# Performance work log

Hardware: AMD Instinct MI355X
Metric: run time of the kernel (lower is better)

## Reference

```python
import jax, jax.numpy as jnp
import numpy as np

NEG_SLOPE = 0.2

def edge_softmax(logits, dst, num_nodes):
    # logits: [E, H]; softmax over incoming edges of each dst node, per head
    m = jax.ops.segment_max(logits, dst, num_segments=num_nodes)  # [N, H]
    e = jnp.exp(logits - m[dst])
    s = jax.ops.segment_sum(e, dst, num_segments=num_nodes)  # [N, H]
    return e / s[dst]

def gat_layer(h, src, dst, W, al, ar, b, activation):
    # W: [F_in, H*D], al/ar: [H, D], b: [H, D]
    N = h.shape[0]
    H, D = al.shape
    feat = (h @ W).reshape(N, H, D)
    el = jnp.sum(feat * al, axis=-1)  # [N, H]
    er = jnp.sum(feat * ar, axis=-1)  # [N, H]
    e = jax.nn.leaky_relu(el[src] + er[dst], NEG_SLOPE)  # [E, H]
    a = edge_softmax(e, dst, N)  # [E, H]
    msg = feat[src] * a[:, :, None]  # [E, H, D]
    rst = jax.ops.segment_sum(msg, dst, num_segments=N) + b[None]  # [N, H, D]
    if activation:
        rst = jax.nn.relu(rst)
    return rst

def setup_inputs() -> dict:
    key = jax.random.key(0)
    ks = jax.random.split(key, 16)
    N, E = 50000, 800000
    IN, HID, OUT, H = 128, 64, 64, 4
    s = 0.1
    return {
        "features": jax.random.normal(ks[0], (N, IN), jnp.float32),
        "src": jax.random.randint(ks[1], (E,), 0, N),
        "dst": jax.random.randint(ks[2], (E,), 0, N),
        "W1": jax.random.normal(ks[3], (IN, H * HID), jnp.float32) * s,
        "al1": jax.random.normal(ks[4], (H, HID), jnp.float32) * s,
        "ar1": jax.random.normal(ks[5], (H, HID), jnp.float32) * s,
        "b1": jnp.zeros((H, HID), jnp.float32),
        "W2": jax.random.normal(ks[6], (H * HID, H * HID), jnp.float32) * s,
        "al2": jax.random.normal(ks[7], (H, HID), jnp.float32) * s,
        "ar2": jax.random.normal(ks[8], (H, HID), jnp.float32) * s,
        "b2": jnp.zeros((H, HID), jnp.float32),
        "W3": jax.random.normal(ks[9], (H * HID, OUT), jnp.float32) * s,
        "al3": jax.random.normal(ks[10], (1, OUT), jnp.float32) * s,
        "ar3": jax.random.normal(ks[11], (1, OUT), jnp.float32) * s,
        "b3": jnp.zeros((1, OUT), jnp.float32),
    }

def reference(features, src, dst, W1, al1, ar1, b1, W2, al2, ar2, b2, W3, al3, ar3, b3):
    N = features.shape[0]
    h = gat_layer(features, src, dst, W1, al1, ar1, b1, activation=True)   # [N, 4, 64]
    h = h.reshape(N, -1)                                                    # [N, 256]
    h = gat_layer(h, src, dst, W2, al2, ar2, b2, activation=True)          # [N, 4, 64]
    h = h.reshape(N, -1)                                                    # [N, 256]
    h = gat_layer(h, src, dst, W3, al3, ar3, b3, activation=False)         # [N, 1, 64]
    return h.mean(axis=1)                                                   # [N, 64]
```

## Files before the change

kernel.cpp:

```cpp
#include <hip/hip_runtime.h>
#include <hip/hip_bf16.h>

#define LEAKY 0.2f
#define LOG2E 1.44269504f

typedef __attribute__((ext_vector_type(8))) short short8;
typedef __attribute__((ext_vector_type(4))) float f32x4;

__device__ inline unsigned short f2b(float f) {
    unsigned u = __float_as_uint(f);
    u += 0x7FFFu + ((u >> 16) & 1u);
    return (unsigned short)(u >> 16);
}
__device__ inline float b2f(unsigned short s) {
    return __uint_as_float(((unsigned)s) << 16);
}
__device__ inline float fexp2(float x) { return __builtin_amdgcn_exp2f(x); }

#define NEB 8192


__global__ __launch_bounds__(256)
void k_prep(const float* __restrict__ features, unsigned short* __restrict__ fconv,
            int n4,
            const float* __restrict__ W1, const float* __restrict__ W2,
            const float* __restrict__ W3, unsigned short* __restrict__ Wt1,
            unsigned short* __restrict__ Wt2, unsigned short* __restrict__ Wt3,
            const int* __restrict__ dst, int* __restrict__ hist, int nbb,
            int E, int N) {
    __shared__ int lc[256];
    const int tid = threadIdx.x;
    if (blockIdx.x < nbb) {
        lc[tid] = 0;
        __syncthreads();
        const int b0 = blockIdx.x * NEB;
        const int cnt = min(NEB, E - b0);
        for (int j = 0; j < NEB / 256; ++j) {
            int idx = j * 256 + tid;
            if (idx < cnt) {
                int dn = dst[b0 + idx];
                if ((unsigned)dn < (unsigned)N) atomicAdd(&lc[dn >> 8], 1);
            }
        }
        __syncthreads();
        hist[blockIdx.x * 256 + tid] = lc[tid];
        return;
    }
    int idx = (blockIdx.x - nbb) * 256 + tid;
    if (idx < n4) {
        float4 v = *(const float4*)(features + idx * 4);
        ushort4 o;
        o.x = f2b(v.x); o.y = f2b(v.y); o.z = f2b(v.z); o.w = f2b(v.w);
        *(ushort4*)(fconv + idx * 4) = o;
        return;
    }
    int j = idx - n4;
    if (j < 32768) {
        int m = j >> 7, k = j & 127;
        Wt1[j] = f2b(W1[(size_t)k * 256 + m]);
        return;
    }
    if (j < 98304) {
        int jj = j - 32768;
        int m = jj >> 8, k = jj & 255;
        Wt2[jj] = f2b(W2[(size_t)k * 256 + m]);
        return;
    }
    if (j < 114688) {
        int jj = j - 98304;
        int m = jj >> 8, k = jj & 255;
        Wt3[jj] = f2b(W3[(size_t)k * 64 + m]);
    }
}


__global__ __launch_bounds__(256)
void k_bucket_scan(const int* __restrict__ hist, int nbb, int* __restrict__ bbase,
                   int* __restrict__ bcur, int* __restrict__ row_start_N, int B, int E) {
    __shared__ int ws[4];
    const int tid = threadIdx.x, lane = tid & 63, wave = tid >> 6;
    int v = 0;
    for (int blk = 0; blk < nbb; ++blk) v += hist[blk * 256 + tid];
    if (tid >= B) v = 0;
    int x = v;
    #pragma unroll
    for (int off = 1; off < 64; off <<= 1) {
        int t = __shfl_up(x, off, 64);
        if (lane >= off) x += t;
    }
    if (lane == 63) ws[wave] = x;
    __syncthreads();
    if (tid == 0) {
        int c = 0;
        #pragma unroll
        for (int wv = 0; wv < 4; ++wv) { int t = ws[wv]; ws[wv] = c; c += t; }
    }
    __syncthreads();
    int excl = x - v + ws[wave];
    if (tid < B) { bbase[tid] = excl; bcur[tid] = excl; }
    if (tid == 0) { bbase[B] = E; *row_start_N = E; }
}

__global__ __launch_bounds__(256)
void k_bin_scatter(const int* __restrict__ dst, int* __restrict__ bcur,
                   int* __restrict__ ebuf, int E, int N) {
    __shared__ int lc[256], lofs[256], lcur[256], gres[256];
    __shared__ int stage_e[NEB];
    __shared__ unsigned short stage_d[NEB];
    __shared__ int ws[4];
    const int tid = threadIdx.x, lane = tid & 63, wave = tid >> 6;
    const int b0 = blockIdx.x * NEB;
    const int cnt = min(NEB, E - b0);
    lc[tid] = 0;
    __syncthreads();

    int dreg[NEB / 256];
    #pragma unroll
    for (int j = 0; j < NEB / 256; ++j) {
        int idx = j * 256 + tid;
        dreg[j] = -1;
        if (idx < cnt) {
            int dn = dst[b0 + idx];
            if ((unsigned)dn < (unsigned)N) {
                dreg[j] = dn;
                atomicAdd(&lc[dn >> 8], 1);
            }
        }
    }
    __syncthreads();
    {
        int v = lc[tid];
        int x = v;
        #pragma unroll
        for (int off = 1; off < 64; off <<= 1) {
            int t = __shfl_up(x, off, 64);
            if (lane >= off) x += t;
        }
        if (lane == 63) ws[wave] = x;
        __syncthreads();
        if (tid == 0) {
            int c = 0;
            #pragma unroll
            for (int wv = 0; wv < 4; ++wv) { int t = ws[wv]; ws[wv] = c; c += t; }
        }
        __syncthreads();
        int excl = x - v + ws[wave];
        lofs[tid] = excl;
        lcur[tid] = excl;
    }
    __syncthreads();
    #pragma unroll
    for (int j = 0; j < NEB / 256; ++j) {
        int dn = dreg[j];
        if (dn >= 0) {
            int p = atomicAdd(&lcur[dn >> 8], 1);
            stage_e[p] = b0 + j * 256 + tid;
            stage_d[p] = (unsigned short)dn;
        }
    }
    __syncthreads();
    if (lc[tid] > 0) gres[tid] = atomicAdd(&bcur[tid], lc[tid]);
    __syncthreads();
    int total = lcur[255];
    for (int i = tid; i < total; i += 256) {
        int dn = stage_d[i];
        int k = dn >> 8;
        int dest = gres[k] + (i - lofs[k]);
        ebuf[dest] = ((dn & 255) << 24) | stage_e[i];
    }
}

__global__ __launch_bounds__(256)
void k_csr_build(const int* __restrict__ ebuf, const int* __restrict__ src,
                 const int* __restrict__ bbase, int* __restrict__ row_start,
                 int* __restrict__ src_sorted, int N) {
    __shared__ int lc[256], lcur[256];
    __shared__ int ws[4];
    const int tid = threadIdx.x, lane = tid & 63, wave = tid >> 6;
    const int k = blockIdx.x;
    const int base = k << 8;
    const int e0 = bbase[k];
    const int cnt = bbase[k + 1] - e0;
    lc[tid] = 0;
    __syncthreads();
    for (int i = tid; i < cnt; i += 256) {
        int rel = ((unsigned)ebuf[e0 + i]) >> 24;
        atomicAdd(&lc[rel], 1);
    }
    __syncthreads();
    {
        int v = lc[tid];
        int x = v;
        #pragma unroll
        for (int off = 1; off < 64; off <<= 1) {
            int t = __shfl_up(x, off, 64);
            if (lane >= off) x += t;
        }
        if (lane == 63) ws[wave] = x;
        __syncthreads();
        if (tid == 0) {
            int c = 0;
            #pragma unroll
            for (int wv = 0; wv < 4; ++wv) { int t = ws[wv]; ws[wv] = c; c += t; }
        }
        __syncthreads();
        int excl = x - v + ws[wave];
        lcur[tid] = excl;
        int n = base + tid;
        if (n < N) row_start[n] = e0 + excl;
    }
    __syncthreads();
    for (int i = tid; i < cnt; i += 256) {
        int val = ebuf[e0 + i];
        int rel = ((unsigned)val) >> 24;
        int e = val & 0xFFFFFF;
        int p = atomicAdd(&lcur[rel], 1);
        src_sorted[e0 + p] = src[e];
    }
}


__global__ __launch_bounds__(256)
void k_gemm_mfma(const unsigned short* __restrict__ A, const unsigned short* __restrict__ Wt,
                 unsigned short* __restrict__ Cb, const float* __restrict__ al,
                 const float* __restrict__ ar, float* __restrict__ el,
                 float* __restrict__ er, int N, int K, int M) {
    constexpr int STR = 40;
    __shared__ unsigned short As[128 * STR];
    __shared__ unsigned short Bs[128 * STR];
    const int tid  = threadIdx.x;
    const int wave = tid >> 6;
    const int lane = tid & 63;
    const int row0 = blockIdx.y * 128;
    const int col0 = blockIdx.x * 128;
    const int wr = (wave >> 1) * 64;
    const int wc = (wave & 1) * 64;
    const int m16 = lane & 15;
    const int q   = lane >> 4;

    const int s_row = tid >> 1;
    const int s_off = (tid & 1) * 16;

    f32x4 acc[4][4] = {};

    for (int k0 = 0; k0 < K; k0 += 32) {
        {
            int gr = row0 + s_row;
            short8 z = {};
            short8 v0 = z, v1 = z;
            if (gr < N) {
                const unsigned short* ap = A + (size_t)gr * K + k0 + s_off;
                v0 = *(const short8*)ap;
                v1 = *(const short8*)(ap + 8);
            }
            *(short8*)&As[s_row * STR + s_off]     = v0;
            *(short8*)&As[s_row * STR + s_off + 8] = v1;
        }
        {
            const unsigned short* sp = Wt + (size_t)(col0 + s_row) * K + k0 + s_off;
            *(short8*)&Bs[s_row * STR + s_off]     = *(const short8*)sp;
            *(short8*)&Bs[s_row * STR + s_off + 8] = *(const short8*)(sp + 8);
        }
        __syncthreads();

        short8 afr[4], bfr[4];
        #pragma unroll
        for (int rg = 0; rg < 4; ++rg)
            afr[rg] = *(const short8*)&As[(wr + rg * 16 + m16) * STR + q * 8];
        #pragma unroll
        for (int cg = 0; cg < 4; ++cg)
            bfr[cg] = *(const short8*)&Bs[(wc + cg * 16 + m16) * STR + q * 8];
        #pragma unroll
        for (int rg = 0; rg < 4; ++rg)
            #pragma unroll
            for (int cg = 0; cg < 4; ++cg)
                acc[rg][cg] = __builtin_amdgcn_mfma_f32_16x16x32_bf16(
                    afr[rg], bfr[cg], acc[rg][cg], 0, 0, 0);
        __syncthreads();
    }

    const int H = M >> 6;
    const int h = (col0 + wc) >> 6;
    float alv[4], arv[4];
    #pragma unroll
    for (int cg = 0; cg < 4; ++cg) {
        alv[cg] = al[h * 64 + cg * 16 + m16];
        arv[cg] = ar[h * 64 + cg * 16 + m16];
    }

    #pragma unroll
    for (int rg = 0; rg < 4; ++rg) {
        #pragma unroll
        for (int r = 0; r < 4; ++r) {
            int gr = row0 + wr + rg * 16 + q * 4 + r;
            float pl = 0.f, pr = 0.f;
            #pragma unroll
            for (int cg = 0; cg < 4; ++cg) {
                pl = fmaf(acc[rg][cg][r], alv[cg], pl);
                pr = fmaf(acc[rg][cg][r], arv[cg], pr);
            }
            #pragma unroll
            for (int off = 1; off < 16; off <<= 1) {
                pl += __shfl_xor(pl, off, 64);
                pr += __shfl_xor(pr, off, 64);
            }
            if (gr < N) {
                unsigned short* bp = Cb + (size_t)gr * M + col0 + wc + m16;
                #pragma unroll
                for (int cg = 0; cg < 4; ++cg)
                    bp[cg * 16] = f2b(acc[rg][cg][r]);
                if (m16 == 0) {
                    el[gr * H + h] = pl * LOG2E;
                    er[gr * H + h] = pr * LOG2E;
                }
            }
        }
    }
}


__global__ __launch_bounds__(256)
void k_gemm_mfma64(const unsigned short* __restrict__ A, const unsigned short* __restrict__ Wt,
                   unsigned short* __restrict__ Cb, const float* __restrict__ al,
                   const float* __restrict__ ar, float* __restrict__ el,
                   float* __restrict__ er, int N, int K) {
    constexpr int M = 64;
    constexpr int STR = 40;
    __shared__ unsigned short As[256 * STR];
    __shared__ unsigned short Bs[64 * STR];
    const int tid  = threadIdx.x;
    const int wave = tid >> 6;
    const int lane = tid & 63;
    const int row0 = blockIdx.x * 256;
    const int wr = wave * 64;
    const int m16 = lane & 15;
    const int q   = lane >> 4;

    const int s_row = tid >> 1;
    const int s_off = (tid & 1) * 16;
    const int b_row = tid >> 2;
    const int b_chk = (tid & 3) * 8;

    f32x4 acc[4][4] = {};

    for (int k0 = 0; k0 < K; k0 += 32) {
        #pragma unroll
        for (int p = 0; p < 2; ++p) {
            int r = s_row + p * 128;
            int gr = row0 + r;
            short8 z = {};
            short8 v0 = z, v1 = z;
            if (gr < N) {
                const unsigned short* ap = A + (size_t)gr * K + k0 + s_off;
                v0 = *(const short8*)ap;
                v1 = *(const short8*)(ap + 8);
            }
            *(short8*)&As[r * STR + s_off]     = v0;
            *(short8*)&As[r * STR + s_off + 8] = v1;
        }
        {
            const unsigned short* sp = Wt + (size_t)b_row * K + k0 + b_chk;
            *(short8*)&Bs[b_row * STR + b_chk] = *(const short8*)sp;
        }
        __syncthreads();

        short8 afr[4], bfr[4];
        #pragma unroll
        for (int rg = 0; rg < 4; ++rg)
            afr[rg] = *(const short8*)&As[(wr + rg * 16 + m16) * STR + q * 8];
        #pragma unroll
        for (int cg = 0; cg < 4; ++cg)
            bfr[cg] = *(const short8*)&Bs[(cg * 16 + m16) * STR + q * 8];
        #pragma unroll
        for (int rg = 0; rg < 4; ++rg)
            #pragma unroll
            for (int cg = 0; cg < 4; ++cg)
                acc[rg][cg] = __builtin_amdgcn_mfma_f32_16x16x32_bf16(
                    afr[rg], bfr[cg], acc[rg][cg], 0, 0, 0);
        __syncthreads();
    }

    float alv[4], arv[4];
    #pragma unroll
    for (int cg = 0; cg < 4; ++cg) {
        alv[cg] = al[cg * 16 + m16];
        arv[cg] = ar[cg * 16 + m16];
    }

    #pragma unroll
    for (int rg = 0; rg < 4; ++rg) {
        #pragma unroll
        for (int r = 0; r < 4; ++r) {
            int gr = row0 + wr + rg * 16 + q * 4 + r;
            float pl = 0.f, pr = 0.f;
            #pragma unroll
            for (int cg = 0; cg < 4; ++cg) {
                pl = fmaf(acc[rg][cg][r], alv[cg], pl);
                pr = fmaf(acc[rg][cg][r], arv[cg], pr);
            }
            #pragma unroll
            for (int off = 1; off < 16; off <<= 1) {
                pl += __shfl_xor(pl, off, 64);
                pr += __shfl_xor(pr, off, 64);
            }
            if (gr < N) {
                unsigned short* bp = Cb + (size_t)gr * M + m16;
                #pragma unroll
                for (int cg = 0; cg < 4; ++cg)
                    bp[cg * 16] = f2b(acc[rg][cg][r]);
                if (m16 == 0) {
                    el[gr] = pl * LOG2E;
                    er[gr] = pr * LOG2E;
                }
            }
        }
    }
}

template<int OUTBF, int HH>
__global__ __launch_bounds__(256)
void k_agg_f(const int* __restrict__ row_start, const int* __restrict__ src_sorted,
             const uint4* __restrict__ featp, const float* __restrict__ el,
             const float* __restrict__ er, const float* __restrict__ bias,
             void* __restrict__ outv, int N, int do_relu) {
    constexpr int M = HH * 64;
    constexpr int P = M >> 3;
    constexpr int G = 256 / P;
    const int grp = threadIdx.x / P;
    const int t = threadIdx.x - grp * P;
    const int n = blockIdx.x * G + grp;
    if (n >= N) return;
    const int d0 = t * 8;
    const int h = d0 >> 6;
    const float erv = er[n * HH + h];

    const int b0 = row_start[n], b1 = row_start[n + 1];

    float a[8] = {};
    float sum = 0.f;
    int i = b0;

    int ssP[8];
    if (i + 8 <= b1) {
        #pragma unroll
        for (int j = 0; j < 8; ++j) ssP[j] = src_sorted[i + j];
    }
    for (; i + 8 <= b1; i += 8) {
        int ss[8];
        #pragma unroll
        for (int j = 0; j < 8; ++j) ss[j] = ssP[j];
        if (i + 16 <= b1) {
            #pragma unroll
            for (int j = 0; j < 8; ++j) ssP[j] = src_sorted[i + 8 + j];
        }
        float wv[8]; uint4 pv[8];
        #pragma unroll
        for (int j = 0; j < 8; ++j) wv[j] = el[(unsigned)(ss[j] * HH + h)];
        #pragma unroll
        for (int j = 0; j < 8; ++j) pv[j] = featp[(unsigned)(ss[j] * P + t)];
        #pragma unroll
        for (int j = 0; j < 8; ++j) {
            float x = wv[j] + erv;
            x = fmaxf(x, LEAKY * x);
            float w = fexp2(x);
            wv[j] = w;
            sum += w;
        }
        #pragma unroll
        for (int j = 0; j < 8; ++j) {
            a[0] = fmaf(__uint_as_float(pv[j].x << 16),         wv[j], a[0]);
            a[1] = fmaf(__uint_as_float(pv[j].x & 0xFFFF0000u), wv[j], a[1]);
            a[2] = fmaf(__uint_as_float(pv[j].y << 16),         wv[j], a[2]);
            a[3] = fmaf(__uint_as_float(pv[j].y & 0xFFFF0000u), wv[j], a[3]);
            a[4] = fmaf(__uint_as_float(pv[j].z << 16),         wv[j], a[4]);
            a[5] = fmaf(__uint_as_float(pv[j].z & 0xFFFF0000u), wv[j], a[5]);
            a[6] = fmaf(__uint_as_float(pv[j].w << 16),         wv[j], a[6]);
            a[7] = fmaf(__uint_as_float(pv[j].w & 0xFFFF0000u), wv[j], a[7]);
        }
    }
    for (; i + 4 <= b1; i += 4) {
        int ss[4]; float wv[4]; uint4 pv[4];
        #pragma unroll
        for (int j = 0; j < 4; ++j) ss[j] = src_sorted[i + j];
        #pragma unroll
        for (int j = 0; j < 4; ++j) wv[j] = el[(unsigned)(ss[j] * HH + h)];
        #pragma unroll
        for (int j = 0; j < 4; ++j) pv[j] = featp[(unsigned)(ss[j] * P + t)];
        #pragma unroll
        for (int j = 0; j < 4; ++j) {
            float x = wv[j] + erv;
            x = fmaxf(x, LEAKY * x);
            float w = fexp2(x);
            wv[j] = w;
            sum += w;
        }
        #pragma unroll
        for (int j = 0; j < 4; ++j) {
            a[0] = fmaf(__uint_as_float(pv[j].x << 16),         wv[j], a[0]);
            a[1] = fmaf(__uint_as_float(pv[j].x & 0xFFFF0000u), wv[j], a[1]);
            a[2] = fmaf(__uint_as_float(pv[j].y << 16),         wv[j], a[2]);
            a[3] = fmaf(__uint_as_float(pv[j].y & 0xFFFF0000u), wv[j], a[3]);
            a[4] = fmaf(__uint_as_float(pv[j].z << 16),         wv[j], a[4]);
            a[5] = fmaf(__uint_as_float(pv[j].z & 0xFFFF0000u), wv[j], a[5]);
            a[6] = fmaf(__uint_as_float(pv[j].w << 16),         wv[j], a[6]);
            a[7] = fmaf(__uint_as_float(pv[j].w & 0xFFFF0000u), wv[j], a[7]);
        }
    }
    for (; i < b1; ++i) {
        int ss = src_sorted[i];
        float x = el[(unsigned)(ss * HH + h)] + erv;
        uint4 pv = featp[(unsigned)(ss * P + t)];
        x = fmaxf(x, LEAKY * x);
        float w = fexp2(x);
        sum += w;
        a[0] = fmaf(__uint_as_float(pv.x << 16),         w, a[0]);
        a[1] = fmaf(__uint_as_float(pv.x & 0xFFFF0000u), w, a[1]);
        a[2] = fmaf(__uint_as_float(pv.y << 16),         w, a[2]);
        a[3] = fmaf(__uint_as_float(pv.y & 0xFFFF0000u), w, a[3]);
        a[4] = fmaf(__uint_as_float(pv.z << 16),         w, a[4]);
        a[5] = fmaf(__uint_as_float(pv.z & 0xFFFF0000u), w, a[5]);
        a[6] = fmaf(__uint_as_float(pv.w << 16),         w, a[6]);
        a[7] = fmaf(__uint_as_float(pv.w & 0xFFFF0000u), w, a[7]);
    }

    float rs = 1.0f / fmaxf(sum, 1e-30f);
    float4 bv0 = *(const float4*)(bias + d0);
    float4 bv1 = *(const float4*)(bias + d0 + 4);
    a[0] = fmaf(a[0], rs, bv0.x); a[1] = fmaf(a[1], rs, bv0.y);
    a[2] = fmaf(a[2], rs, bv0.z); a[3] = fmaf(a[3], rs, bv0.w);
    a[4] = fmaf(a[4], rs, bv1.x); a[5] = fmaf(a[5], rs, bv1.y);
    a[6] = fmaf(a[6], rs, bv1.z); a[7] = fmaf(a[7], rs, bv1.w);
    if (do_relu) {
        #pragma unroll
        for (int j = 0; j < 8; ++j) a[j] = fmaxf(a[j], 0.f);
    }
    if (OUTBF) {
        uint4 o;
        o.x = (unsigned)f2b(a[0]) | ((unsigned)f2b(a[1]) << 16);
        o.y = (unsigned)f2b(a[2]) | ((unsigned)f2b(a[3]) << 16);
        o.z = (unsigned)f2b(a[4]) | ((unsigned)f2b(a[5]) << 16);
        o.w = (unsigned)f2b(a[6]) | ((unsigned)f2b(a[7]) << 16);
        *(uint4*)((unsigned short*)outv + (size_t)n * M + d0) = o;
    } else {
        *(float4*)((float*)outv + (size_t)n * M + d0)     = make_float4(a[0], a[1], a[2], a[3]);
        *(float4*)((float*)outv + (size_t)n * M + d0 + 4) = make_float4(a[4], a[5], a[6], a[7]);
    }
}


static void run_layer(const unsigned short* A, int K, const unsigned short* Wt,
                      const float* al_, const float* ar_, const float* b_, int H,
                      unsigned short* featb, void* rstOut, bool outBf,
                      float* el, float* er,
                      const int* row_start, const int* src_sorted,
                      int N, int E, bool do_relu, hipStream_t stream) {
    const int M = H * 64;
    if (M % 128 == 0) {
        dim3 gg(M / 128, (N + 127) / 128);
        k_gemm_mfma<<<gg, 256, 0, stream>>>(A, Wt, featb, al_, ar_, el, er, N, K, M);
    } else {
        k_gemm_mfma64<<<(N + 255) / 256, 256, 0, stream>>>(A, Wt, featb, al_, ar_, el, er, N, K);
    }

    int G = 256 / (M / 8);
    int blocks = (N + G - 1) / G;
    if (H == 4) {
        if (outBf)
            k_agg_f<1, 4><<<blocks, 256, 0, stream>>>(row_start, src_sorted,
                                                      (const uint4*)featb, el, er,
                                                      b_, rstOut, N, do_relu ? 1 : 0);
        else
            k_agg_f<0, 4><<<blocks, 256, 0, stream>>>(row_start, src_sorted,
                                                      (const uint4*)featb, el, er,
                                                      b_, rstOut, N, do_relu ? 1 : 0);
    } else {
        if (outBf)
            k_agg_f<1, 1><<<blocks, 256, 0, stream>>>(row_start, src_sorted,
                                                      (const uint4*)featb, el, er,
                                                      b_, rstOut, N, do_relu ? 1 : 0);
        else
            k_agg_f<0, 1><<<blocks, 256, 0, stream>>>(row_start, src_sorted,
                                                      (const uint4*)featb, el, er,
                                                      b_, rstOut, N, do_relu ? 1 : 0);
    }
}

extern "C" void kernel_launch(void* const* d_in, const int* in_sizes, int n_in,
                              void* d_out, int out_size, void* d_ws, size_t ws_size,
                              hipStream_t stream) {
    const float* features = (const float*)d_in[0];
    const int*   src = (const int*)d_in[1];
    const int*   dst = (const int*)d_in[2];
    const float* W1  = (const float*)d_in[3];
    const float* al1 = (const float*)d_in[4];
    const float* ar1 = (const float*)d_in[5];
    const float* b1  = (const float*)d_in[6];
    const float* W2  = (const float*)d_in[7];
    const float* al2 = (const float*)d_in[8];
    const float* ar2 = (const float*)d_in[9];
    const float* b2  = (const float*)d_in[10];
    const float* W3  = (const float*)d_in[11];
    const float* al3 = (const float*)d_in[12];
    const float* ar3 = (const float*)d_in[13];
    const float* b3  = (const float*)d_in[14];

    const int N = in_sizes[0] / 128;
    const int E = in_sizes[1];
    const int B = (N + 255) >> 8;
    const int n4 = N * 128 / 4;
    const int nbb = (E + NEB - 1) / NEB;

    float* ws   = (float*)d_ws;
    float* el   = ws;
    float* er   = el + (size_t)N * 4;
    int* row_start  = (int*)(er + (size_t)N * 4);
    int* src_sorted = row_start + N + 1;
    int* ebuf       = src_sorted + E;
    int* bbase      = ebuf + E;
    int* bcur       = bbase + 257;
    int* hist       = bcur + 256;
    uintptr_t wp = (uintptr_t)(hist + (size_t)nbb * 256);
    wp = (wp + 15) & ~(uintptr_t)15;
    unsigned short* Wt1   = (unsigned short*)wp;
    unsigned short* Wt2   = Wt1 + 32768;
    unsigned short* Wt3   = Wt2 + 65536;
    unsigned short* fconv = Wt3 + 16384;
    unsigned short* featb = fconv + (size_t)N * 128;
    unsigned short* rstb  = featb + (size_t)N * 256;

    int prep_total = n4 + 114688;
    int prep_blocks = nbb + (prep_total + 255) / 256;
    k_prep<<<prep_blocks, 256, 0, stream>>>(features, fconv, n4,
                                            W1, W2, W3, Wt1, Wt2, Wt3,
                                            dst, hist, nbb, E, N);

    k_bucket_scan<<<1, 256, 0, stream>>>(hist, nbb, bbase, bcur, row_start + N, B, E);
    k_bin_scatter<<<nbb, 256, 0, stream>>>(dst, bcur, ebuf, E, N);
    k_csr_build<<<B, 256, 0, stream>>>(ebuf, src, bbase, row_start, src_sorted, N);

    run_layer(fconv, 128, Wt1, al1, ar1, b1, 4, featb, rstb, true,
              el, er, row_start, src_sorted, N, E, true, stream);
    run_layer(rstb, 256, Wt2, al2, ar2, b2, 4, featb, rstb, true,
              el, er, row_start, src_sorted, N, E, true, stream);
    run_layer(rstb, 256, Wt3, al3, ar3, b3, 1, featb, d_out, false,
              el, er, row_start, src_sorted, N, E, false, stream);
}
```

Before: 395.8 us.

## Permute feature column layout so GEMM epilogue writes packed ushort4 stores

The GEMM epilogue now stores each lane's four column-group outputs as one contiguous ushort4 instead of four scattered 2-byte stores, which gives a permuted column order in the intermediate feature buffers. Downstream consumers are adjusted to match: the next layers' weights are pre-permuted along K, and the aggregation kernel reads bias and writes fp32 output with the inverse permutation. The aim is to cut the cost of narrow global writes in the GEMM. In exchange, bias loads become scalar gathers and the final fp32 output uses strided float2 stores.

```diff
diff --git a/kernel.cpp b/kernel.cpp
--- a/kernel.cpp
+++ b/kernel.cpp
@@ -18,6 +18,7 @@
 __device__ inline float fexp2(float x) { return __builtin_amdgcn_exp2f(x); }
 
 #define NEB 8192
+
 
 
 __global__ __launch_bounds__(256)
@@ -62,14 +63,16 @@
     }
     if (j < 98304) {
         int jj = j - 32768;
-        int m = jj >> 8, k = jj & 255;
-        Wt2[jj] = f2b(W2[(size_t)k * 256 + m]);
+        int m = jj >> 8, ks = jj & 255;
+        int kt = (ks & 192) | ((ks & 3) << 4) | ((ks & 63) >> 2);
+        Wt2[jj] = f2b(W2[(size_t)kt * 256 + m]);
         return;
     }
     if (j < 114688) {
         int jj = j - 98304;
-        int m = jj >> 8, k = jj & 255;
-        Wt3[jj] = f2b(W3[(size_t)k * 64 + m]);
+        int m = jj >> 8, ks = jj & 255;
+        int kt = (ks & 192) | ((ks & 3) << 4) | ((ks & 63) >> 2);
+        Wt3[jj] = f2b(W3[(size_t)kt * 64 + m]);
     }
 }
 
@@ -305,10 +308,10 @@
                 pr += __shfl_xor(pr, off, 64);
             }
             if (gr < N) {
-                unsigned short* bp = Cb + (size_t)gr * M + col0 + wc + m16;
-                #pragma unroll
-                for (int cg = 0; cg < 4; ++cg)
-                    bp[cg * 16] = f2b(acc[rg][cg][r]);
+                ushort4 o;
+                o.x = f2b(acc[rg][0][r]); o.y = f2b(acc[rg][1][r]);
+                o.z = f2b(acc[rg][2][r]); o.w = f2b(acc[rg][3][r]);
+                *(ushort4*)(Cb + (size_t)gr * M + (col0 + wc) + m16 * 4) = o;
                 if (m16 == 0) {
                     el[gr * H + h] = pl * LOG2E;
                     er[gr * H + h] = pr * LOG2E;
@@ -404,10 +407,10 @@
                 pr += __shfl_xor(pr, off, 64);
             }
             if (gr < N) {
-                unsigned short* bp = Cb + (size_t)gr * M + m16;
-                #pragma unroll
-                for (int cg = 0; cg < 4; ++cg)
-                    bp[cg * 16] = f2b(acc[rg][cg][r]);
+                ushort4 o;
+                o.x = f2b(acc[rg][0][r]); o.y = f2b(acc[rg][1][r]);
+                o.z = f2b(acc[rg][2][r]); o.w = f2b(acc[rg][3][r]);
+                *(ushort4*)(Cb + (size_t)gr * M + m16 * 4) = o;
                 if (m16 == 0) {
                     el[gr] = pl * LOG2E;
                     er[gr] = pr * LOG2E;
@@ -524,12 +527,11 @@
     }
 
     float rs = 1.0f / fmaxf(sum, 1e-30f);
-    float4 bv0 = *(const float4*)(bias + d0);
-    float4 bv1 = *(const float4*)(bias + d0 + 4);
-    a[0] = fmaf(a[0], rs, bv0.x); a[1] = fmaf(a[1], rs, bv0.y);
-    a[2] = fmaf(a[2], rs, bv0.z); a[3] = fmaf(a[3], rs, bv0.w);
-    a[4] = fmaf(a[4], rs, bv1.x); a[5] = fmaf(a[5], rs, bv1.y);
-    a[6] = fmaf(a[6], rs, bv1.z); a[7] = fmaf(a[7], rs, bv1.w);
+    const int c0 = (d0 & 63) >> 2;
+    const float* bh = bias + h * 64 + c0;
+    #pragma unroll
+    for (int j = 0; j < 8; ++j)
+        a[j] = fmaf(a[j], rs, bh[16 * (j & 3) + (j >> 2)]);
     if (do_relu) {
         #pragma unroll
         for (int j = 0; j < 8; ++j) a[j] = fmaxf(a[j], 0.f);
@@ -542,8 +544,10 @@
         o.w = (unsigned)f2b(a[6]) | ((unsigned)f2b(a[7]) << 16);
         *(uint4*)((unsigned short*)outv + (size_t)n * M + d0) = o;
     } else {
-        *(float4*)((float*)outv + (size_t)n * M + d0)     = make_float4(a[0], a[1], a[2], a[3]);
-        *(float4*)((float*)outv + (size_t)n * M + d0 + 4) = make_float4(a[4], a[5], a[6], a[7]);
+        float* op = (float*)outv + (size_t)n * M + h * 64 + c0;
+        #pragma unroll
+        for (int j = 0; j < 4; ++j)
+            *(float2*)(op + 16 * j) = make_float2(a[j], a[j + 4]);
     }
 }
 
```

After: 391.7 us. Within noise of the previous version (-1.0%).
